# Kernel optimization log

Measured on AMD Instinct MI355X. Metric: run time of the kernel, lower is better.

## Reference

```python
import jax, jax.numpy as jnp
import numpy as np

P_DROP = 0.2
N_NODES = 100000
N_EDGES = 1600000
IN_DIM, HID_DIM, OUT_DIM = 128, 128, 64


def sage_conv(x, src, dst, Wl, Wr, b, n_nodes):
    # PyG SAGEConv (aggr='mean', root_weight=True):
    #   out_i = W_l @ mean_{j in N(i)} x_j + W_r @ x_i + b
    msgs = jnp.take(x, src, axis=0)                                   # [E, d]
    agg = jax.ops.segment_sum(msgs, dst, num_segments=n_nodes)        # [N, d]
    cnt = jax.ops.segment_sum(jnp.ones((src.shape[0],), x.dtype), dst,
                              num_segments=n_nodes)                   # [N]
    agg = agg / jnp.maximum(cnt, 1.0)[:, None]                        # mean, 0 for isolated nodes
    return agg @ Wl + x @ Wr + b


def setup_inputs() -> dict:
    key = jax.random.key(0)
    ks = jax.random.split(key, 8)
    x = jax.random.normal(ks[0], (N_NODES, IN_DIM), dtype=jnp.float32)
    edge_index = jax.random.randint(ks[1], (2, N_EDGES), 0, N_NODES, dtype=jnp.int32)
    drop_u = jax.random.uniform(ks[2], (N_NODES, HID_DIM), dtype=jnp.float32)
    s1 = 1.0 / np.sqrt(IN_DIM)
    s2 = 1.0 / np.sqrt(HID_DIM)
    W1l = jax.random.normal(ks[3], (IN_DIM, HID_DIM), dtype=jnp.float32) * s1
    W1r = jax.random.normal(ks[4], (IN_DIM, HID_DIM), dtype=jnp.float32) * s1
    b1 = jnp.zeros((HID_DIM,), dtype=jnp.float32)
    W2l = jax.random.normal(ks[5], (HID_DIM, OUT_DIM), dtype=jnp.float32) * s2
    W2r = jax.random.normal(ks[6], (HID_DIM, OUT_DIM), dtype=jnp.float32) * s2
    b2 = jnp.zeros((OUT_DIM,), dtype=jnp.float32)
    return {"x": x, "edge_index": edge_index, "drop_u": drop_u,
            "W1l": W1l, "W1r": W1r, "b1": b1,
            "W2l": W2l, "W2r": W2r, "b2": b2}


def reference(x, edge_index, drop_u, W1l, W1r, b1, W2l, W2r, b2):
    n = x.shape[0]
    src, dst = edge_index[0], edge_index[1]
    h = jax.nn.elu(sage_conv(x, src, dst, W1l, W1r, b1, n))
    keep = (drop_u >= P_DROP).astype(h.dtype) / (1.0 - P_DROP)  # inverted dropout, p=0.2
    h = h * keep
    h = jax.nn.elu(sage_conv(h, src, dst, W2l, W2r, b2, n))
    return h
```

## Files before the change

kernel.cpp:

```cpp
#include <hip/hip_runtime.h>
#include <cstdint>
#include <cstddef>

#define TPB 256
#define BCAP 2560
#define NBKMAX 800
#define EPB 8192

typedef short bf16x8 __attribute__((ext_vector_type(8)));
typedef float f32x4 __attribute__((ext_vector_type(4)));

__device__ __forceinline__ unsigned short f2bf(float f) {
  unsigned int u = __float_as_uint(f);
  unsigned int r = (u + 0x7fffu + ((u >> 16) & 1u)) >> 16;
  return (unsigned short)r;
}
__device__ __forceinline__ float bf2f(unsigned short h) {
  return __uint_as_float(((unsigned int)h) << 16);
}

__device__ __forceinline__ void gload16(const void* g, void* l) {
  __builtin_amdgcn_global_load_lds(
      (const __attribute__((address_space(1))) unsigned int*)g,
      (__attribute__((address_space(3))) unsigned int*)l, 16, 0, 0);
}

template <int N>
__device__ __forceinline__ void waitvm() {
  asm volatile("s_waitcnt vmcnt(%0)" ::"n"(N) : "memory");
}


__global__ __launch_bounds__(256) void multisplit_scatter(
    const int* __restrict__ src, const int* __restrict__ dst,
    unsigned int* __restrict__ be, int* __restrict__ bcnt, int e, int nbk) {
  __shared__ int hist[NBKMAX];
  __shared__ int curs[NBKMAX];
  int tx = threadIdx.x;
  int e0 = blockIdx.x * EPB;
  int e1 = min(e, e0 + EPB);

  for (int b = tx; b < nbk; b += TPB) hist[b] = 0;
  __syncthreads();
  for (int i = e0 + tx; i < e1; i += TPB) atomicAdd(&hist[dst[i] >> 7], 1);
  __syncthreads();
  int rot = (blockIdx.x * 131) % nbk;
  for (int s = tx; s < nbk; s += TPB) {
    int b = s + rot;
    if (b >= nbk) b -= nbk;
    int h = hist[b];
    curs[b] = (h > 0) ? atomicAdd(&bcnt[b], h) : 0;
  }
  __syncthreads();
  for (int i = e0 + tx; i < e1; i += TPB) {
    int d = dst[i];
    int b = d >> 7;
    int p = atomicAdd(&curs[b], 1);
    if (p < BCAP)
      be[(size_t)b * BCAP + p] = ((unsigned int)(d & 127) << 17) | (unsigned int)src[i];
  }
}

__global__ void bucket_scan(const int* __restrict__ bcnt, int* __restrict__ bbase, int nbk) {
  __shared__ int s[TPB];
  __shared__ int carry;
  int tx = threadIdx.x;
  if (tx == 0) carry = 0;
  __syncthreads();
  for (int base = 0; base < nbk; base += TPB) {
    int i = base + tx;
    int v = (i < nbk) ? bcnt[i] : 0;
    s[tx] = v;
    __syncthreads();
    for (int d = 1; d < TPB; d <<= 1) {
      int t = (tx >= d) ? s[tx - d] : 0;
      __syncthreads();
      s[tx] += t;
      __syncthreads();
    }
    int c = carry;
    if (i < nbk) bbase[i] = c + s[tx] - v;
    __syncthreads();
    if (tx == TPB - 1) carry = c + s[tx];
    __syncthreads();
  }
}

__global__ __launch_bounds__(256) void per_bucket_build(
    const unsigned int* __restrict__ be, const int* __restrict__ bcnt,
    const int* __restrict__ bbase, int* __restrict__ off, int* __restrict__ col,
    int n, int e) {
  int b = blockIdx.x, tx = threadIdx.x;
  int cnt = bcnt[b];
  if (cnt > BCAP) cnt = BCAP;
  int base = bbase[b];
  int node0 = b << 7;
  __shared__ int scnt[128];
  __shared__ int sscan[128];
  if (tx < 128) scnt[tx] = 0;
  __syncthreads();
  const unsigned int* eb = be + (size_t)b * BCAP;
  for (int i = tx; i < cnt; i += 256) atomicAdd(&scnt[eb[i] >> 17], 1);
  __syncthreads();
  if (tx < 128) sscan[tx] = scnt[tx];
  __syncthreads();
  for (int d = 1; d < 128; d <<= 1) {
    int t = 0;
    if (tx < 128 && tx >= d) t = sscan[tx - d];
    __syncthreads();
    if (tx < 128) sscan[tx] += t;
    __syncthreads();
  }
  if (tx < 128) {
    int excl = sscan[tx] - scnt[tx];
    if (node0 + tx < n) off[node0 + tx] = base + excl;
    scnt[tx] = excl;
  }
  if (b == 0 && tx == 0) off[n] = e;
  __syncthreads();
  for (int i = tx; i < cnt; i += 256) {
    unsigned int u = eb[i];
    int p = atomicAdd(&scnt[u >> 17], 1);
    col[base + p] = (int)(u & 0x1ffff);
  }
}


__global__ void f32_to_bf16_v4(const float* __restrict__ in, unsigned short* __restrict__ out,
                               int n4) {
  int i = blockIdx.x * TPB + threadIdx.x;
  if (i >= n4) return;
  float4 v = ((const float4*)in)[i];
  ushort4 o;
  o.x = f2bf(v.x); o.y = f2bf(v.y); o.z = f2bf(v.z); o.w = f2bf(v.w);
  ((ushort4*)out)[i] = o;
}

__global__ void make_dropmask(const float* __restrict__ u, unsigned char* __restrict__ m,
                              int n4) {
  int i = blockIdx.x * TPB + threadIdx.x;
  if (i >= n4) return;
  float4 v = ((const float4*)u)[i];
  uchar4 o;
  o.x = (v.x >= 0.2f) ? 1 : 0;
  o.y = (v.y >= 0.2f) ? 1 : 0;
  o.z = (v.z >= 0.2f) ? 1 : 0;
  o.w = (v.w >= 0.2f) ? 1 : 0;
  ((uchar4*)m)[i] = o;
}

template <int NF>
__global__ void build_wt(const float* __restrict__ Wl, const float* __restrict__ Wr,
                         unsigned short* __restrict__ Wt) {
  int idx = blockIdx.x * TPB + threadIdx.x;
  if (idx >= NF * 256) return;
  int nn = idx >> 8;
  int k = idx & 255;
  float v = (k < 128) ? Wl[k * NF + nn] : Wr[(k - 128) * NF + nn];
  Wt[idx] = f2bf(v);
}

__global__ void build_wt2p(const float* __restrict__ W2l, const float* __restrict__ W2r,
                           unsigned short* __restrict__ Wt) {
  int idx = blockIdx.x * TPB + threadIdx.x;
  if (idx >= 128 * 128) return;
  int nn = idx >> 7;
  int k = idx & 127;
  float v = (nn < 64) ? W2l[k * 64 + nn] : W2r[k * 64 + (nn - 64)];
  Wt[idx] = f2bf(v);
}


__global__ void aggregate_bf(const unsigned short* __restrict__ X,
                             const int* __restrict__ off, const int* __restrict__ col,
                             unsigned short* __restrict__ out, int n) {
  int wv = (blockIdx.x * TPB + threadIdx.x) >> 6;
  int lane = threadIdx.x & 63;
  int li = lane & 15;
  int node = wv * 4 + (lane >> 4);
  if (node >= n) return;
  int s0 = off[node], s1 = off[node + 1];
  int cnt = s1 - s0;

  float a0 = 0.f, a1 = 0.f, a2 = 0.f, a3 = 0.f,
        a4 = 0.f, a5 = 0.f, a6 = 0.f, a7 = 0.f;

  for (int base = 0; base < cnt; base += 16) {
    int idx = s0 + base + li;
    int ci = col[min(idx, s1 - 1)];
    int lim = cnt - base;
#pragma unroll
    for (int j = 0; j < 16; ++j) {
      int c = __shfl(ci, j, 16);
      const uint4* p = (const uint4*)(X + (size_t)c * 128 + li * 8);
      uint4 v = *p;
      float s = (j < lim) ? 1.f : 0.f;
      a0 = fmaf(s, __uint_as_float(v.x << 16), a0);
      a1 = fmaf(s, __uint_as_float(v.x & 0xffff0000u), a1);
      a2 = fmaf(s, __uint_as_float(v.y << 16), a2);
      a3 = fmaf(s, __uint_as_float(v.y & 0xffff0000u), a3);
      a4 = fmaf(s, __uint_as_float(v.z << 16), a4);
      a5 = fmaf(s, __uint_as_float(v.z & 0xffff0000u), a5);
      a6 = fmaf(s, __uint_as_float(v.w << 16), a6);
      a7 = fmaf(s, __uint_as_float(v.w & 0xffff0000u), a7);
    }
  }

  float inv = (cnt > 0) ? 1.0f / (float)cnt : 0.f;
  uint4 o;
  o.x = ((unsigned int)f2bf(a1 * inv) << 16) | f2bf(a0 * inv);
  o.y = ((unsigned int)f2bf(a3 * inv) << 16) | f2bf(a2 * inv);
  o.z = ((unsigned int)f2bf(a5 * inv) << 16) | f2bf(a4 * inv);
  o.w = ((unsigned int)f2bf(a7 * inv) << 16) | f2bf(a6 * inv);
  *(uint4*)(out + (size_t)node * 128 + li * 8) = o;
}


__global__ void aggregate_add(const unsigned short* __restrict__ P,
                              const int* __restrict__ off, const int* __restrict__ col,
                              const float* __restrict__ Q, float* __restrict__ out, int n) {
  int wv = (blockIdx.x * TPB + threadIdx.x) >> 6;
  int lane = threadIdx.x & 63;
  int li = lane & 7;
  int node = wv * 8 + (lane >> 3);
  bool alive = node < n;
  int s0 = 0, s1 = 0;
  if (alive) { s0 = off[node]; s1 = off[node + 1]; }
  int cnt = s1 - s0;

  float a0 = 0.f, a1 = 0.f, a2 = 0.f, a3 = 0.f,
        a4 = 0.f, a5 = 0.f, a6 = 0.f, a7 = 0.f;

  for (int base = 0; base < cnt; base += 8) {
    int ci = col[max(0, min(s0 + base + li, s1 - 1))];
    int lim = cnt - base;
#pragma unroll
    for (int j = 0; j < 8; ++j) {
      int c = __shfl(ci, j, 8);
      uint4 v = *(const uint4*)(P + (size_t)c * 64 + li * 8);
      float s = (j < lim) ? 1.f : 0.f;
      a0 = fmaf(s, __uint_as_float(v.x << 16), a0);
      a1 = fmaf(s, __uint_as_float(v.x & 0xffff0000u), a1);
      a2 = fmaf(s, __uint_as_float(v.y << 16), a2);
      a3 = fmaf(s, __uint_as_float(v.y & 0xffff0000u), a3);
      a4 = fmaf(s, __uint_as_float(v.z << 16), a4);
      a5 = fmaf(s, __uint_as_float(v.z & 0xffff0000u), a5);
      a6 = fmaf(s, __uint_as_float(v.w << 16), a6);
      a7 = fmaf(s, __uint_as_float(v.w & 0xffff0000u), a7);
    }
  }

  if (alive) {
    float inv = (cnt > 0) ? 1.0f / (float)cnt : 0.f;
    const float4* qp = (const float4*)(Q + (size_t)node * 64 + li * 8);
    float4 q0 = qp[0], q1 = qp[1];
    float4 o0, o1;
    o0.x = a0 * inv + q0.x; o0.y = a1 * inv + q0.y;
    o0.z = a2 * inv + q0.z; o0.w = a3 * inv + q0.w;
    o1.x = a4 * inv + q1.x; o1.y = a5 * inv + q1.y;
    o1.z = a6 * inv + q1.z; o1.w = a7 * inv + q1.w;
    o0.x = (o0.x > 0.f) ? o0.x : expm1f(o0.x);
    o0.y = (o0.y > 0.f) ? o0.y : expm1f(o0.y);
    o0.z = (o0.z > 0.f) ? o0.z : expm1f(o0.z);
    o0.w = (o0.w > 0.f) ? o0.w : expm1f(o0.w);
    o1.x = (o1.x > 0.f) ? o1.x : expm1f(o1.x);
    o1.y = (o1.y > 0.f) ? o1.y : expm1f(o1.y);
    o1.z = (o1.z > 0.f) ? o1.z : expm1f(o1.z);
    o1.w = (o1.w > 0.f) ? o1.w : expm1f(o1.w);
    float4* op = (float4*)(out + (size_t)node * 64 + li * 8);
    op[0] = o0; op[1] = o1;
  }
}


template <int NCH, int MODE>
__global__ __launch_bounds__(256) void gemm_mfma(
    const unsigned short* __restrict__ A1, const unsigned short* __restrict__ A2,
    const unsigned short* __restrict__ Wt, const float* __restrict__ bias,
    const unsigned char* __restrict__ dmask, unsigned short* __restrict__ outb,
    float* __restrict__ outf, int n) {
  constexpr int IPC = 6;
  constexpr int KTOT = NCH * 64;
  __shared__ __align__(16) unsigned short sA[2][128 * 64];
  __shared__ __align__(16) unsigned short sB[2][64 * 64];

  int g = blockIdx.x;
  int p = (g >> 4) * 8 + (g & 7);
  int yy = (g >> 3) & 1;
  int nrb = (n + 127) >> 7;
  if (p >= nrb) return;

  int tid = threadIdx.x;
  int row0 = p * 128;
  int ncol0 = yy * 64;
  int lane = tid & 63;
  int wid = tid >> 6;
  int wm = wid >> 1, wn = wid & 1;
  int lq = lane & 15, q = lane >> 4;

  int sr = tid >> 3, sc8 = tid & 7;
  int cg = sc8 ^ (sr & 7);

  int arow[4];
#pragma unroll
  for (int t = 0; t < 4; ++t) arow[t] = min(row0 + sr + t * 32, n - 1);

  f32x4 acc[4][2];
#pragma unroll
  for (int i = 0; i < 4; ++i)
#pragma unroll
    for (int j = 0; j < 2; ++j) acc[i][j] = (f32x4)(0.f);

  auto issue = [&](int c, int b) {
    const unsigned short* Asrc = (c < 2) ? A1 : A2;
    int koff = (c & 1) * 64;
#pragma unroll
    for (int t = 0; t < 4; ++t) {
      gload16(Asrc + (size_t)arow[t] * 128 + koff + cg * 8,
              (char*)sA[b] + t * 4096 + wid * 1024);
    }
#pragma unroll
    for (int t = 0; t < 2; ++t) {
      gload16(Wt + (size_t)(ncol0 + sr + t * 32) * KTOT + c * 64 + cg * 8,
              (char*)sB[b] + t * 4096 + wid * 1024);
    }
  };

  issue(0, 0);
  issue(1, 1);

#pragma unroll
  for (int c = 0; c < NCH; ++c) {
    if (c < NCH - 1) waitvm<IPC>(); else waitvm<0>();
    __builtin_amdgcn_s_barrier();
    __builtin_amdgcn_sched_barrier(0);

    const int buf = c & 1;
#pragma unroll
    for (int ks = 0; ks < 2; ++ks) {
      bf16x8 a[4], b[2];
#pragma unroll
      for (int i = 0; i < 4; ++i) {
        int rr = wm * 64 + i * 16 + lq;
        a[i] = *(const bf16x8*)(&sA[buf][rr * 64 + (((ks * 4 + q) ^ (rr & 7)) * 8)]);
      }
#pragma unroll
      for (int j = 0; j < 2; ++j) {
        int rb = wn * 32 + j * 16 + lq;
        b[j] = *(const bf16x8*)(&sB[buf][rb * 64 + (((ks * 4 + q) ^ (rb & 7)) * 8)]);
      }
#pragma unroll
      for (int i = 0; i < 4; ++i)
#pragma unroll
        for (int j = 0; j < 2; ++j)
          acc[i][j] = __builtin_amdgcn_mfma_f32_16x16x32_bf16(a[i], b[j], acc[i][j], 0, 0, 0);
    }

    if (c < NCH - 2) {
      asm volatile("s_waitcnt lgkmcnt(0)" ::: "memory");
      __builtin_amdgcn_sched_barrier(0);
      __builtin_amdgcn_s_barrier();
      issue(c + 2, buf);
    }
  }

#pragma unroll
  for (int j = 0; j < 2; ++j) {
    int gcol = ncol0 + wn * 32 + j * 16 + lq;
    float bv;
    if (MODE == 0) bv = bias[gcol];
    else bv = (gcol >= 64) ? bias[gcol - 64] : 0.f;
#pragma unroll
    for (int i = 0; i < 4; ++i) {
      int rbase = row0 + wm * 64 + i * 16 + q * 4;
#pragma unroll
      for (int r = 0; r < 4; ++r) {
        int row = rbase + r;
        if (row >= n) continue;
        float v = acc[i][j][r] + bv;
        if (MODE == 0) {
          v = (v > 0.f) ? v : expm1f(v);
          unsigned char k = dmask[(size_t)row * 128 + gcol];
          v = k ? v * 1.25f : 0.f;
          outb[(size_t)row * 128 + gcol] = f2bf(v);
        } else {
          if (gcol < 64) outb[(size_t)row * 64 + gcol] = f2bf(v);
          else outf[(size_t)row * 64 + (gcol - 64)] = v;
        }
      }
    }
  }
}


extern "C" void kernel_launch(void* const* d_in, const int* in_sizes, int n_in,
                              void* d_out, int out_size, void* d_ws, size_t ws_size,
                              hipStream_t stream) {
  const float* x = (const float*)d_in[0];
  const int* ei = (const int*)d_in[1];
  const float* dropu = (const float*)d_in[2];
  const float* W1l = (const float*)d_in[3];
  const float* W1r = (const float*)d_in[4];
  const float* b1 = (const float*)d_in[5];
  const float* W2l = (const float*)d_in[6];
  const float* W2r = (const float*)d_in[7];
  const float* b2 = (const float*)d_in[8];

  int n = in_sizes[0] / 128;
  int e = in_sizes[1] / 2;
  const int* src = ei;
  const int* dst = ei + e;
  float* out = (float*)d_out;

  char* w = (char*)d_ws;
  auto alloc = [&](size_t bytes) -> char* {
    char* p = w;
    w += (bytes + 255) & ~(size_t)255;
    return p;
  };
  int nbk = (n + 127) / 128;
  int* off = (int*)alloc((size_t)(n + 1) * sizeof(int));
  int* col = (int*)alloc((size_t)e * sizeof(int));
  int* bcnt = (int*)alloc((size_t)nbk * sizeof(int));
  int* bbase = (int*)alloc((size_t)nbk * sizeof(int));
  unsigned short* xb = (unsigned short*)alloc((size_t)n * 128 * 2);
  unsigned short* hb = (unsigned short*)alloc((size_t)n * 128 * 2);
  unsigned short* aggb = (unsigned short*)alloc((size_t)n * 128 * 2);
  unsigned char* dmask = (unsigned char*)alloc((size_t)n * 128);
  unsigned short* Wt1 = (unsigned short*)alloc(128 * 256 * 2);
  unsigned short* Wt2 = (unsigned short*)alloc(128 * 128 * 2);
  unsigned int* be = (unsigned int*)aggb;
  unsigned short* pb = xb;
  float* qf = (float*)aggb;

  hipMemsetAsync(bcnt, 0, (size_t)nbk * sizeof(int), stream);

  int gMS = (e + EPB - 1) / EPB;
  multisplit_scatter<<<gMS, TPB, 0, stream>>>(src, dst, be, bcnt, e, nbk);
  bucket_scan<<<1, TPB, 0, stream>>>(bcnt, bbase, nbk);
  per_bucket_build<<<nbk, TPB, 0, stream>>>(be, bcnt, bbase, off, col, n, e);

  int n4 = n * 128 / 4;
  f32_to_bf16_v4<<<(n4 + TPB - 1) / TPB, TPB, 0, stream>>>(x, xb, n4);
  make_dropmask<<<(n4 + TPB - 1) / TPB, TPB, 0, stream>>>(dropu, dmask, n4);
  build_wt<128><<<(128 * 256 + TPB - 1) / TPB, TPB, 0, stream>>>(W1l, W1r, Wt1);
  build_wt2p<<<(128 * 128 + TPB - 1) / TPB, TPB, 0, stream>>>(W2l, W2r, Wt2);

  int gAgg1 = ((n + 3) / 4 * 64 + TPB - 1) / TPB;
  int gAgg2 = (n + 31) / 32;
  int gR = (n + 127) / 128;
  int gG = ((gR + 7) / 8) * 16;

  aggregate_bf<<<gAgg1, TPB, 0, stream>>>(xb, off, col, aggb, n);
  gemm_mfma<4, 0><<<gG, TPB, 0, stream>>>(aggb, xb, Wt1, b1, dmask, hb, nullptr, n);

  gemm_mfma<2, 1><<<gG, TPB, 0, stream>>>(hb, nullptr, Wt2, b2, nullptr, pb, qf, n);
  aggregate_add<<<gAgg2, TPB, 0, stream>>>(pb, off, col, qf, out, n);
}
```

Measured before the change: 404.3 us.

## Drop bucket scan via atomic base, shrink GEMM row tile, use fast exp for ELU

Removes the single-block bucket_scan kernel. Each per-bucket block now claims its base offset with an atomicAdd on a global cursor and writes explicit end offsets, so the CSR segments are no longer laid out in order. The MFMA GEMM row tile is halved from 128 to 64, which doubles the grid and cuts shared memory per block, and the A-chunk indexing is generalised. ELU's expm1f is replaced by __expf(v)-1, a cheaper call that loses some precision near zero.

```diff
diff --git a/kernel.cpp b/kernel.cpp
--- a/kernel.cpp
+++ b/kernel.cpp
@@ -18,6 +18,8 @@
 __device__ __forceinline__ float bf2f(unsigned short h) {
   return __uint_as_float(((unsigned int)h) << 16);
 }
+
+__device__ __forceinline__ float elu_neg(float v) { return __expf(v) - 1.0f; }
 
 __device__ __forceinline__ void gload16(const void* g, void* l) {
   __builtin_amdgcn_global_load_lds(
@@ -61,42 +63,17 @@
   }
 }
 
-__global__ void bucket_scan(const int* __restrict__ bcnt, int* __restrict__ bbase, int nbk) {
-  __shared__ int s[TPB];
-  __shared__ int carry;
-  int tx = threadIdx.x;
-  if (tx == 0) carry = 0;
-  __syncthreads();
-  for (int base = 0; base < nbk; base += TPB) {
-    int i = base + tx;
-    int v = (i < nbk) ? bcnt[i] : 0;
-    s[tx] = v;
-    __syncthreads();
-    for (int d = 1; d < TPB; d <<= 1) {
-      int t = (tx >= d) ? s[tx - d] : 0;
-      __syncthreads();
-      s[tx] += t;
-      __syncthreads();
-    }
-    int c = carry;
-    if (i < nbk) bbase[i] = c + s[tx] - v;
-    __syncthreads();
-    if (tx == TPB - 1) carry = c + s[tx];
-    __syncthreads();
-  }
-}
-
 __global__ __launch_bounds__(256) void per_bucket_build(
     const unsigned int* __restrict__ be, const int* __restrict__ bcnt,
-    const int* __restrict__ bbase, int* __restrict__ off, int* __restrict__ col,
-    int n, int e) {
+    int* __restrict__ gcur, int* __restrict__ off, int* __restrict__ offend,
+    int* __restrict__ col, int n) {
   int b = blockIdx.x, tx = threadIdx.x;
   int cnt = bcnt[b];
   if (cnt > BCAP) cnt = BCAP;
-  int base = bbase[b];
   int node0 = b << 7;
   __shared__ int scnt[128];
   __shared__ int sscan[128];
+  __shared__ int sbase;
   if (tx < 128) scnt[tx] = 0;
   __syncthreads();
   const unsigned int* eb = be + (size_t)b * BCAP;
@@ -111,12 +88,17 @@
     if (tx < 128) sscan[tx] += t;
     __syncthreads();
   }
+  if (tx == 0) sbase = atomicAdd(gcur, cnt);
+  __syncthreads();
+  int base = sbase;
   if (tx < 128) {
     int excl = sscan[tx] - scnt[tx];
-    if (node0 + tx < n) off[node0 + tx] = base + excl;
+    if (node0 + tx < n) {
+      off[node0 + tx] = base + excl;
+      offend[node0 + tx] = base + sscan[tx];
+    }
     scnt[tx] = excl;
   }
-  if (b == 0 && tx == 0) off[n] = e;
   __syncthreads();
   for (int i = tx; i < cnt; i += 256) {
     unsigned int u = eb[i];
@@ -172,14 +154,15 @@
 
 
 __global__ void aggregate_bf(const unsigned short* __restrict__ X,
-                             const int* __restrict__ off, const int* __restrict__ col,
+                             const int* __restrict__ off, const int* __restrict__ offend,
+                             const int* __restrict__ col,
                              unsigned short* __restrict__ out, int n) {
   int wv = (blockIdx.x * TPB + threadIdx.x) >> 6;
   int lane = threadIdx.x & 63;
   int li = lane & 15;
   int node = wv * 4 + (lane >> 4);
   if (node >= n) return;
-  int s0 = off[node], s1 = off[node + 1];
+  int s0 = off[node], s1 = offend[node];
   int cnt = s1 - s0;
 
   float a0 = 0.f, a1 = 0.f, a2 = 0.f, a3 = 0.f,
@@ -217,7 +200,8 @@
 
 
 __global__ void aggregate_add(const unsigned short* __restrict__ P,
-                              const int* __restrict__ off, const int* __restrict__ col,
+                              const int* __restrict__ off, const int* __restrict__ offend,
+                              const int* __restrict__ col,
                               const float* __restrict__ Q, float* __restrict__ out, int n) {
   int wv = (blockIdx.x * TPB + threadIdx.x) >> 6;
   int lane = threadIdx.x & 63;
@@ -225,7 +209,7 @@
   int node = wv * 8 + (lane >> 3);
   bool alive = node < n;
   int s0 = 0, s1 = 0;
-  if (alive) { s0 = off[node]; s1 = off[node + 1]; }
+  if (alive) { s0 = off[node]; s1 = offend[node]; }
   int cnt = s1 - s0;
 
   float a0 = 0.f, a1 = 0.f, a2 = 0.f, a3 = 0.f,
@@ -259,14 +243,14 @@
     o0.z = a2 * inv + q0.z; o0.w = a3 * inv + q0.w;
     o1.x = a4 * inv + q1.x; o1.y = a5 * inv + q1.y;
     o1.z = a6 * inv + q1.z; o1.w = a7 * inv + q1.w;
-    o0.x = (o0.x > 0.f) ? o0.x : expm1f(o0.x);
-    o0.y = (o0.y > 0.f) ? o0.y : expm1f(o0.y);
-    o0.z = (o0.z > 0.f) ? o0.z : expm1f(o0.z);
-    o0.w = (o0.w > 0.f) ? o0.w : expm1f(o0.w);
-    o1.x = (o1.x > 0.f) ? o1.x : expm1f(o1.x);
-    o1.y = (o1.y > 0.f) ? o1.y : expm1f(o1.y);
-    o1.z = (o1.z > 0.f) ? o1.z : expm1f(o1.z);
-    o1.w = (o1.w > 0.f) ? o1.w : expm1f(o1.w);
+    o0.x = (o0.x > 0.f) ? o0.x : elu_neg(o0.x);
+    o0.y = (o0.y > 0.f) ? o0.y : elu_neg(o0.y);
+    o0.z = (o0.z > 0.f) ? o0.z : elu_neg(o0.z);
+    o0.w = (o0.w > 0.f) ? o0.w : elu_neg(o0.w);
+    o1.x = (o1.x > 0.f) ? o1.x : elu_neg(o1.x);
+    o1.y = (o1.y > 0.f) ? o1.y : elu_neg(o1.y);
+    o1.z = (o1.z > 0.f) ? o1.z : elu_neg(o1.z);
+    o1.w = (o1.w > 0.f) ? o1.w : elu_neg(o1.w);
     float4* op = (float4*)(out + (size_t)node * 64 + li * 8);
     op[0] = o0; op[1] = o1;
   }
@@ -279,19 +263,19 @@
     const unsigned short* __restrict__ Wt, const float* __restrict__ bias,
     const unsigned char* __restrict__ dmask, unsigned short* __restrict__ outb,
     float* __restrict__ outf, int n) {
-  constexpr int IPC = 6;
+  constexpr int IPC = 4;
   constexpr int KTOT = NCH * 64;
-  __shared__ __align__(16) unsigned short sA[2][128 * 64];
+  __shared__ __align__(16) unsigned short sA[2][64 * 64];
   __shared__ __align__(16) unsigned short sB[2][64 * 64];
 
   int g = blockIdx.x;
   int p = (g >> 4) * 8 + (g & 7);
   int yy = (g >> 3) & 1;
-  int nrb = (n + 127) >> 7;
+  int nrb = (n + 63) >> 6;
   if (p >= nrb) return;
 
   int tid = threadIdx.x;
-  int row0 = p * 128;
+  int row0 = p * 64;
   int ncol0 = yy * 64;
   int lane = tid & 63;
   int wid = tid >> 6;
@@ -301,21 +285,21 @@
   int sr = tid >> 3, sc8 = tid & 7;
   int cg = sc8 ^ (sr & 7);
 
-  int arow[4];
-#pragma unroll
-  for (int t = 0; t < 4; ++t) arow[t] = min(row0 + sr + t * 32, n - 1);
-
-  f32x4 acc[4][2];
-#pragma unroll
-  for (int i = 0; i < 4; ++i)
+  int arow[2];
+#pragma unroll
+  for (int t = 0; t < 2; ++t) arow[t] = min(row0 + sr + t * 32, n - 1);
+
+  f32x4 acc[2][2];
+#pragma unroll
+  for (int i = 0; i < 2; ++i)
 #pragma unroll
     for (int j = 0; j < 2; ++j) acc[i][j] = (f32x4)(0.f);
 
   auto issue = [&](int c, int b) {
-    const unsigned short* Asrc = (c < 2) ? A1 : A2;
-    int koff = (c & 1) * 64;
-#pragma unroll
-    for (int t = 0; t < 4; ++t) {
+    const unsigned short* Asrc = (MODE == 0 && c >= NCH / 2) ? A2 : A1;
+    int koff = (MODE == 0 ? (c & (NCH / 2 - 1)) : c) * 64;
+#pragma unroll
+    for (int t = 0; t < 2; ++t) {
       gload16(Asrc + (size_t)arow[t] * 128 + koff + cg * 8,
               (char*)sA[b] + t * 4096 + wid * 1024);
     }
@@ -338,10 +322,10 @@
     const int buf = c & 1;
 #pragma unroll
     for (int ks = 0; ks < 2; ++ks) {
-      bf16x8 a[4], b[2];
-#pragma unroll
-      for (int i = 0; i < 4; ++i) {
-        int rr = wm * 64 + i * 16 + lq;
+      bf16x8 a[2], b[2];
+#pragma unroll
+      for (int i = 0; i < 2; ++i) {
+        int rr = wm * 32 + i * 16 + lq;
         a[i] = *(const bf16x8*)(&sA[buf][rr * 64 + (((ks * 4 + q) ^ (rr & 7)) * 8)]);
       }
 #pragma unroll
@@ -350,7 +334,7 @@
         b[j] = *(const bf16x8*)(&sB[buf][rb * 64 + (((ks * 4 + q) ^ (rb & 7)) * 8)]);
       }
 #pragma unroll
-      for (int i = 0; i < 4; ++i)
+      for (int i = 0; i < 2; ++i)
 #pragma unroll
         for (int j = 0; j < 2; ++j)
           acc[i][j] = __builtin_amdgcn_mfma_f32_16x16x32_bf16(a[i], b[j], acc[i][j], 0, 0, 0);
@@ -371,15 +355,15 @@
     if (MODE == 0) bv = bias[gcol];
     else bv = (gcol >= 64) ? bias[gcol - 64] : 0.f;
 #pragma unroll
-    for (int i = 0; i < 4; ++i) {
-      int rbase = row0 + wm * 64 + i * 16 + q * 4;
+    for (int i = 0; i < 2; ++i) {
+      int rbase = row0 + wm * 32 + i * 16 + q * 4;
 #pragma unroll
       for (int r = 0; r < 4; ++r) {
         int row = rbase + r;
         if (row >= n) continue;
         float v = acc[i][j][r] + bv;
         if (MODE == 0) {
-          v = (v > 0.f) ? v : expm1f(v);
+          v = (v > 0.f) ? v : elu_neg(v);
           unsigned char k = dmask[(size_t)row * 128 + gcol];
           v = k ? v * 1.25f : 0.f;
           outb[(size_t)row * 128 + gcol] = f2bf(v);
@@ -419,10 +403,11 @@
     return p;
   };
   int nbk = (n + 127) / 128;
-  int* off = (int*)alloc((size_t)(n + 1) * sizeof(int));
+  int* off = (int*)alloc((size_t)n * sizeof(int));
+  int* offend = (int*)alloc((size_t)n * sizeof(int));
   int* col = (int*)alloc((size_t)e * sizeof(int));
-  int* bcnt = (int*)alloc((size_t)nbk * sizeof(int));
-  int* bbase = (int*)alloc((size_t)nbk * sizeof(int));
+  int* bcnt = (int*)alloc((size_t)(nbk + 1) * sizeof(int));
+  int* gcur = bcnt + nbk;
   unsigned short* xb = (unsigned short*)alloc((size_t)n * 128 * 2);
   unsigned short* hb = (unsigned short*)alloc((size_t)n * 128 * 2);
   unsigned short* aggb = (unsigned short*)alloc((size_t)n * 128 * 2);
@@ -433,12 +418,11 @@
   unsigned short* pb = xb;
   float* qf = (float*)aggb;
 
-  hipMemsetAsync(bcnt, 0, (size_t)nbk * sizeof(int), stream);
+  hipMemsetAsync(bcnt, 0, (size_t)(nbk + 1) * sizeof(int), stream);
 
   int gMS = (e + EPB - 1) / EPB;
   multisplit_scatter<<<gMS, TPB, 0, stream>>>(src, dst, be, bcnt, e, nbk);
-  bucket_scan<<<1, TPB, 0, stream>>>(bcnt, bbase, nbk);
-  per_bucket_build<<<nbk, TPB, 0, stream>>>(be, bcnt, bbase, off, col, n, e);
+  per_bucket_build<<<nbk, TPB, 0, stream>>>(be, bcnt, gcur, off, offend, col, n);
 
   int n4 = n * 128 / 4;
   f32_to_bf16_v4<<<(n4 + TPB - 1) / TPB, TPB, 0, stream>>>(x, xb, n4);
@@ -448,12 +432,12 @@
 
   int gAgg1 = ((n + 3) / 4 * 64 + TPB - 1) / TPB;
   int gAgg2 = (n + 31) / 32;
-  int gR = (n + 127) / 128;
+  int gR = (n + 63) / 64;
   int gG = ((gR + 7) / 8) * 16;
 
-  aggregate_bf<<<gAgg1, TPB, 0, stream>>>(xb, off, col, aggb, n);
+  aggregate_bf<<<gAgg1, TPB, 0, stream>>>(xb, off, offend, col, aggb, n);
   gemm_mfma<4, 0><<<gG, TPB, 0, stream>>>(aggb, xb, Wt1, b1, dmask, hb, nullptr, n);
 
   gemm_mfma<2, 1><<<gG, TPB, 0, stream>>>(hb, nullptr, Wt2, b2, nullptr, pb, qf, n);
-  aggregate_add<<<gAgg2, TPB, 0, stream>>>(pb, off, col, qf, out, n);
-}
+  aggregate_add<<<gAgg2, TPB, 0, stream>>>(pb, off, offend, col, qf, out, n);
+}
```

New measurement: 382.2 us. 5.5% less time.
